# Kernel optimization log

Hardware: AMD Instinct MI355X
Metric: run time of the kernel (lower is better)

Reference implementation:

```python
import jax, jax.numpy as jnp
import numpy as np

N_HEADS = 16
DIM_HEAD = 64
ROPE_THETA = 10000.0


def _rope_tables(seq_len, dim_head, dtype):
    # [N, dim_head//2] angle tables, llama-style interleaved-pair rotation
    inv_freq = 1.0 / (ROPE_THETA ** (jnp.arange(0, dim_head, 2, dtype=jnp.float32) / dim_head))
    t = jnp.arange(seq_len, dtype=jnp.float32)
    freqs = jnp.outer(t, inv_freq)  # [N, D/2]
    return jnp.cos(freqs).astype(dtype), jnp.sin(freqs).astype(dtype)


def _apply_rope(x, cos, sin):
    # x: [B, H, N, D]; rotate interleaved pairs (x[2i], x[2i+1])
    xr = x[..., 0::2]
    xi = x[..., 1::2]
    cos = cos[None, None, :, :]
    sin = sin[None, None, :, :]
    out_r = xr * cos - xi * sin
    out_i = xr * sin + xi * cos
    return jnp.stack([out_r, out_i], axis=-1).reshape(x.shape)


def _l2norm(x, eps=1e-12):
    return x / jnp.maximum(jnp.linalg.norm(x, axis=-1, keepdims=True), eps)


def setup_inputs() -> dict:
    key = jax.random.key(0)
    ks = jax.random.split(key, 5)
    B, N, dim = 1, 4096, N_HEADS * DIM_HEAD
    q = jax.random.normal(ks[0], (B, N, dim), dtype=jnp.float32)
    k = jax.random.normal(ks[1], (B, N, dim), dtype=jnp.float32)
    v = jax.random.normal(ks[2], (B, N, dim), dtype=jnp.float32)
    qk_scale = jnp.full((1, 1, 1, DIM_HEAD), 10.0, dtype=jnp.float32)
    w_out = jax.random.normal(ks[3], (dim, dim), dtype=jnp.float32) * (dim ** -0.5)
    b_out = jnp.zeros((dim,), dtype=jnp.float32)
    return {"q": q, "k": k, "v": v, "qk_scale": qk_scale, "w_out": w_out, "b_out": b_out}


def reference(q, k, v, qk_scale, w_out, b_out):
    B, N, dim = q.shape
    H, D = N_HEADS, DIM_HEAD
    scale = D ** -0.5
    # [B, N, dim] -> [B, H, N, D]
    q = q.reshape(B, N, H, D).transpose(0, 2, 1, 3)
    k = k.reshape(B, N, H, D).transpose(0, 2, 1, 3)
    v = v.reshape(B, N, H, D).transpose(0, 2, 1, 3)
    # RoPE
    cos, sin = _rope_tables(N, D, q.dtype)
    q = _apply_rope(q, cos, sin)
    k = _apply_rope(k, cos, sin)
    # QK-norm: L2-normalize then learned scale
    q = _l2norm(q) * qk_scale
    k = _l2norm(k) * qk_scale
    # explicit attention (non-flash)
    scores = jnp.einsum('bhid,bhjd->bhij', q, k) * scale
    probs = jax.nn.softmax(scores, axis=-1)
    out = jnp.einsum('bhij,bhjd->bhid', probs, v)
    out = out.transpose(0, 2, 1, 3).reshape(B, N, dim)
    # Linear: y = x W^T + b
    return out @ w_out.T + b_out
```

## Files before the change

kernel.cpp:

```cpp
#include <hip/hip_runtime.h>
#include <hip/hip_bf16.h>

#define N_CTX 4096
#define NH    16
#define DH    64
#define DIM   1024
#define NSPLIT 2
#define KT_PER_SPLIT (N_CTX / 64 / NSPLIT)

typedef __attribute__((ext_vector_type(8))) short bf16x8;
typedef __attribute__((ext_vector_type(4))) float f32x4;

__device__ __forceinline__ ushort f2bf(float f) {
    union { float f; unsigned u; } x; x.f = f;
    unsigned r = (x.u + 0x7FFFu + ((x.u >> 16) & 1u)) >> 16;
    return (ushort)r;
}
__device__ __forceinline__ unsigned fbits(float f) {
    union { float f; unsigned u; } x; x.f = f; return x.u;
}
__device__ __forceinline__ unsigned pack_bf16(float lo, float hi) {
    unsigned a = fbits(lo) + 0x8000u;
    unsigned b = fbits(hi) + 0x8000u;
#if defined(__has_builtin)
#if __has_builtin(__builtin_amdgcn_perm)
    return __builtin_amdgcn_perm(b, a, 0x07060302u);
#else
    return (a >> 16) | (b & 0xFFFF0000u);
#endif
#else
    return (a >> 16) | (b & 0xFFFF0000u);
#endif
}
__device__ __forceinline__ float fast_exp2(float x) {
#if defined(__has_builtin)
#if __has_builtin(__builtin_amdgcn_exp2f)
    return __builtin_amdgcn_exp2f(x);
#else
    return exp2f(x);
#endif
#else
    return exp2f(x);
#endif
}

#define SC 0.18033688011112042f

__global__ __launch_bounds__(256) void prep_kernel(
    const float* __restrict__ x, const float* __restrict__ qk_scale,
    ushort* __restrict__ xb, float premul)
{
    const int lane = threadIdx.x & 63;
    const int wave = threadIdx.x >> 6;
    const int row  = blockIdx.x * 4 + wave;
    const int n = row >> 4;
    const int h = row & 15;

    float val = x[(size_t)n * DIM + h * DH + lane];
    float other = __shfl_xor(val, 1, 64);

    const int i = lane >> 1;
    float inv_freq = 1.0f / powf(10000.0f, (float)i * (1.0f / 32.0f));
    float ang = (float)n * inv_freq;
    float s, c;
    sincosf(ang, &s, &c);

    float r = (lane & 1) ? fmaf(other, s, val * c)
                         : fmaf(val, c, -(other * s));

    float ss = r * r;
    #pragma unroll
    for (int off = 32; off > 0; off >>= 1)
        ss += __shfl_xor(ss, off, 64);
    float invn = 1.0f / fmaxf(sqrtf(ss), 1e-12f);
    float scl  = qk_scale[lane] * premul;

    xb[((size_t)h * N_CTX + n) * DH + lane] = f2bf(r * invn * scl);
}

__global__ __launch_bounds__(256) void vtrans_kernel(
    const float* __restrict__ v, ushort* __restrict__ vt)
{
    __shared__ ushort L[64][68];
    const int kt = blockIdx.x, h = blockIdx.y, t = threadIdx.x;

    for (int e = t; e < 4096; e += 256) {
        int key = e >> 6, d = e & 63;
        float f = v[(size_t)(kt * 64 + key) * DIM + h * DH + d];
        L[d][key] = f2bf(f);
    }
    __syncthreads();
    for (int e = t; e < 4096; e += 256) {
        int d = e >> 6, key = e & 63;
        vt[((size_t)h * DH + d) * N_CTX + kt * 64 + key] = L[d][key];
    }
}

__global__ __launch_bounds__(256) void wconv_kernel(
    const float* __restrict__ w, ushort* __restrict__ wb)
{
    int i = (blockIdx.x * 256 + threadIdx.x) * 4;
    float4 f = *(const float4*)&w[i];
    ushort4 u;
    u.x = f2bf(f.x); u.y = f2bf(f.y); u.z = f2bf(f.z); u.w = f2bf(f.w);
    *(ushort4*)&wb[i] = u;
}

__global__ __launch_bounds__(256) void attn_kernel(
    const ushort* __restrict__ qb, const ushort* __restrict__ kb,
    const ushort* __restrict__ vt, float* __restrict__ opart,
    float* __restrict__ lpart)
{
    __shared__ ushort Ks[64][72];
    __shared__ ushort Vt[64][72];
    __shared__ ushort Ps[128][72];

    const int h     = blockIdx.y;
    const int qbase = blockIdx.x * 128;
    const int sp    = blockIdx.z;
    const int kbase = sp * (N_CTX / NSPLIT);
    const int t    = threadIdx.x;
    const int w    = t >> 6;
    const int lane = t & 63;
    const int l15  = lane & 15;
    const int quad = lane >> 4;

    bf16x8 qf[2][2];
    #pragma unroll
    for (int qt = 0; qt < 2; qt++) {
        const size_t qrow = ((size_t)h * N_CTX + qbase + w * 32 + qt * 16 + l15) * DH;
        qf[qt][0] = *(const bf16x8*)&qb[qrow + quad * 8];
        qf[qt][1] = *(const bf16x8*)&qb[qrow + 32 + quad * 8];
    }

    float l_part[2] = {0.0f, 0.0f};
    f32x4 o_acc[4][2];
    #pragma unroll
    for (int dt = 0; dt < 4; dt++)
        #pragma unroll
        for (int qt = 0; qt < 2; qt++)
            o_acc[dt][qt] = (f32x4){0.f, 0.f, 0.f, 0.f};

    const int sr = t >> 3;
    const int sc = (t & 7) * 8;
    const ushort* kp0 = &kb[((size_t)h * N_CTX + kbase + sr) * DH + sc];
    const ushort* kp1 = kp0 + (size_t)32 * DH;
    const ushort* vp0 = &vt[((size_t)h * DH + sr) * N_CTX + kbase + sc];
    const ushort* vp1 = vp0 + (size_t)32 * N_CTX;
    bf16x8 kr0 = *(const bf16x8*)kp0, kr1 = *(const bf16x8*)kp1;
    bf16x8 vr0 = *(const bf16x8*)vp0, vr1 = *(const bf16x8*)vp1;

    for (int kt = 0; kt < KT_PER_SPLIT; kt++) {
        __syncthreads();
        *(bf16x8*)&Ks[sr][sc]      = kr0;
        *(bf16x8*)&Ks[sr + 32][sc] = kr1;
        *(bf16x8*)&Vt[sr][sc]      = vr0;
        *(bf16x8*)&Vt[sr + 32][sc] = vr1;
        __syncthreads();
        if (kt + 1 < KT_PER_SPLIT) {
            kr0 = *(const bf16x8*)(kp0 + (size_t)(kt + 1) * 64 * DH);
            kr1 = *(const bf16x8*)(kp1 + (size_t)(kt + 1) * 64 * DH);
            vr0 = *(const bf16x8*)(vp0 + (size_t)(kt + 1) * 64);
            vr1 = *(const bf16x8*)(vp1 + (size_t)(kt + 1) * 64);
        }

        #pragma unroll
        for (int j = 0; j < 4; j++) {
            bf16x8 kf0 = *(const bf16x8*)&Ks[j * 16 + l15][quad * 8];
            bf16x8 kf1 = *(const bf16x8*)&Ks[j * 16 + l15][32 + quad * 8];
            f32x4 s0 = (f32x4){0.f, 0.f, 0.f, 0.f};
            f32x4 s1 = (f32x4){0.f, 0.f, 0.f, 0.f};
            s0 = __builtin_amdgcn_mfma_f32_16x16x32_bf16(kf0, qf[0][0], s0, 0, 0, 0);
            s1 = __builtin_amdgcn_mfma_f32_16x16x32_bf16(kf0, qf[1][0], s1, 0, 0, 0);
            s0 = __builtin_amdgcn_mfma_f32_16x16x32_bf16(kf1, qf[0][1], s0, 0, 0, 0);
            s1 = __builtin_amdgcn_mfma_f32_16x16x32_bf16(kf1, qf[1][1], s1, 0, 0, 0);

            {
                float p0 = fast_exp2(s0.x), p1 = fast_exp2(s0.y);
                float p2 = fast_exp2(s0.z), p3 = fast_exp2(s0.w);
                l_part[0] += (p0 + p1) + (p2 + p3);
                uint2 pk; pk.x = pack_bf16(p0, p1); pk.y = pack_bf16(p2, p3);
                *(uint2*)&Ps[w * 32 + l15][j * 16 + quad * 4] = pk;
            }
            {
                float p0 = fast_exp2(s1.x), p1 = fast_exp2(s1.y);
                float p2 = fast_exp2(s1.z), p3 = fast_exp2(s1.w);
                l_part[1] += (p0 + p1) + (p2 + p3);
                uint2 pk; pk.x = pack_bf16(p0, p1); pk.y = pack_bf16(p2, p3);
                *(uint2*)&Ps[w * 32 + 16 + l15][j * 16 + quad * 4] = pk;
            }
        }

        #pragma unroll
        for (int ks = 0; ks < 2; ks++) {
            bf16x8 pf0 = *(const bf16x8*)&Ps[w * 32 + l15][ks * 32 + quad * 8];
            bf16x8 pf1 = *(const bf16x8*)&Ps[w * 32 + 16 + l15][ks * 32 + quad * 8];
            #pragma unroll
            for (int dt = 0; dt < 4; dt++) {
                bf16x8 vf = *(const bf16x8*)&Vt[dt * 16 + l15][ks * 32 + quad * 8];
                o_acc[dt][0] = __builtin_amdgcn_mfma_f32_16x16x32_bf16(vf, pf0, o_acc[dt][0], 0, 0, 0);
                o_acc[dt][1] = __builtin_amdgcn_mfma_f32_16x16x32_bf16(vf, pf1, o_acc[dt][1], 0, 0, 0);
            }
        }
    }

    #pragma unroll
    for (int qt = 0; qt < 2; qt++) {
        float v = l_part[qt];
        v += __shfl_xor(v, 16, 64);
        v += __shfl_xor(v, 32, 64);
        if (quad == 0)
            lpart[(size_t)sp * NH * N_CTX + (size_t)h * N_CTX
                  + qbase + w * 32 + qt * 16 + l15] = v;
    }

    #pragma unroll
    for (int qt = 0; qt < 2; qt++)
        #pragma unroll
        for (int dt = 0; dt < 4; dt++) {
            f32x4 o = o_acc[dt][qt];
            float4 ov; ov.x = o.x; ov.y = o.y; ov.z = o.z; ov.w = o.w;
            *(float4*)&opart[((size_t)sp * N_CTX + qbase + w * 32 + qt * 16 + l15) * DIM
                             + h * DH + dt * 16 + quad * 4] = ov;
        }
}

__global__ __launch_bounds__(256) void combine_kernel(
    const float* __restrict__ opart, const float* __restrict__ lpart,
    ushort* __restrict__ attnb)
{
    const int idx = blockIdx.x * 256 + threadIdx.x;
    const int n   = idx >> 8;
    const int rem = idx & 255;
    const int h   = rem >> 4;
    const size_t e = (size_t)n * DIM + h * DH + (rem & 15) * 4;

    float4 o0 = *(const float4*)&opart[e];
    float4 o1 = *(const float4*)&opart[(size_t)N_CTX * DIM + e];
    float l0 = lpart[(size_t)h * N_CTX + n];
    float l1 = lpart[(size_t)NH * N_CTX + (size_t)h * N_CTX + n];
    float li = 1.0f / (l0 + l1);

    ushort4 r;
    r.x = f2bf((o0.x + o1.x) * li);
    r.y = f2bf((o0.y + o1.y) * li);
    r.z = f2bf((o0.z + o1.z) * li);
    r.w = f2bf((o0.w + o1.w) * li);
    *(ushort4*)&attnb[e] = r;
}

__global__ __launch_bounds__(256) void proj_kernel(
    const ushort* __restrict__ A, const ushort* __restrict__ W,
    const float* __restrict__ bias, float* __restrict__ out)
{
    __shared__ ushort As[128][72];
    __shared__ ushort Ws[64][72];

    const int nbase = blockIdx.x * 128;
    const int obase = blockIdx.y * 64;
    const int t    = threadIdx.x;
    const int w    = t >> 6;
    const int lane = t & 63;
    const int l15  = lane & 15;
    const int quad = lane >> 4;
    const int rw   = (w >> 1) * 64;
    const int cw   = (w & 1) * 32;

    f32x4 acc[4][2];
    #pragma unroll
    for (int mt = 0; mt < 4; mt++)
        #pragma unroll
        for (int nt = 0; nt < 2; nt++)
            acc[mt][nt] = (f32x4){0.f, 0.f, 0.f, 0.f};

    for (int kt = 0; kt < DIM / 64; kt++) {
        const int kb = kt * 64;
        __syncthreads();
        #pragma unroll
        for (int i = 0; i < 4; i++) {
            int c = t + i * 256, r = c >> 3, c8 = c & 7;
            *(bf16x8*)&As[r][c8 * 8] =
                *(const bf16x8*)&A[(size_t)(nbase + r) * DIM + kb + c8 * 8];
        }
        #pragma unroll
        for (int i = 0; i < 2; i++) {
            int c = t + i * 256, r = c >> 3, c8 = c & 7;
            *(bf16x8*)&Ws[r][c8 * 8] =
                *(const bf16x8*)&W[(size_t)(obase + r) * DIM + kb + c8 * 8];
        }
        __syncthreads();

        bf16x8 af[4][2], bfr[2][2];
        #pragma unroll
        for (int mt = 0; mt < 4; mt++)
            #pragma unroll
            for (int kh = 0; kh < 2; kh++)
                af[mt][kh] = *(const bf16x8*)&As[rw + mt * 16 + l15][kh * 32 + quad * 8];
        #pragma unroll
        for (int nt = 0; nt < 2; nt++)
            #pragma unroll
            for (int kh = 0; kh < 2; kh++)
                bfr[nt][kh] = *(const bf16x8*)&Ws[cw + nt * 16 + l15][kh * 32 + quad * 8];

        #pragma unroll
        for (int mt = 0; mt < 4; mt++)
            #pragma unroll
            for (int nt = 0; nt < 2; nt++) {
                acc[mt][nt] = __builtin_amdgcn_mfma_f32_16x16x32_bf16(af[mt][0], bfr[nt][0], acc[mt][nt], 0, 0, 0);
                acc[mt][nt] = __builtin_amdgcn_mfma_f32_16x16x32_bf16(af[mt][1], bfr[nt][1], acc[mt][nt], 0, 0, 0);
            }
    }

    #pragma unroll
    for (int nt = 0; nt < 2; nt++) {
        int o = obase + cw + nt * 16 + l15;
        float bb = bias[o];
        #pragma unroll
        for (int mt = 0; mt < 4; mt++) {
            int nrow = nbase + rw + mt * 16 + quad * 4;
            out[(size_t)(nrow + 0) * DIM + o] = acc[mt][nt].x + bb;
            out[(size_t)(nrow + 1) * DIM + o] = acc[mt][nt].y + bb;
            out[(size_t)(nrow + 2) * DIM + o] = acc[mt][nt].z + bb;
            out[(size_t)(nrow + 3) * DIM + o] = acc[mt][nt].w + bb;
        }
    }
}

extern "C" void kernel_launch(void* const* d_in, const int* in_sizes, int n_in,
                              void* d_out, int out_size, void* d_ws, size_t ws_size,
                              hipStream_t stream)
{
    const float* q        = (const float*)d_in[0];
    const float* k        = (const float*)d_in[1];
    const float* v        = (const float*)d_in[2];
    const float* qk_scale = (const float*)d_in[3];
    const float* w_out    = (const float*)d_in[4];
    const float* b_out    = (const float*)d_in[5];
    float* out = (float*)d_out;

    const size_t per = (size_t)NH * N_CTX * DH;
    ushort* qb    = (ushort*)d_ws;
    ushort* kb    = qb + per;
    ushort* vtg   = kb + per;
    ushort* attnb = vtg + per;
    ushort* wb    = attnb + per;
    float*  opart = (float*)(wb + (size_t)DIM * DIM);
    float*  lpart = opart + (size_t)NSPLIT * N_CTX * DIM;

    prep_kernel<<<dim3(N_CTX * NH / 4), 256, 0, stream>>>(q, qk_scale, qb, SC);
    prep_kernel<<<dim3(N_CTX * NH / 4), 256, 0, stream>>>(k, qk_scale, kb, 1.0f);
    vtrans_kernel<<<dim3(N_CTX / 64, NH), 256, 0, stream>>>(v, vtg);
    wconv_kernel<<<dim3(DIM * DIM / 1024), 256, 0, stream>>>(w_out, wb);
    attn_kernel<<<dim3(N_CTX / 128, NH, NSPLIT), 256, 0, stream>>>(qb, kb, vtg, opart, lpart);
    combine_kernel<<<dim3(N_CTX * DIM / 4 / 256), 256, 0, stream>>>(opart, lpart, attnb);
    proj_kernel<<<dim3(N_CTX / 128, DIM / 64), 256, 0, stream>>>(attnb, wb, b_out, out);
}
```

Measured before the change: 262.3 us.

## Load K fragments directly from global, quadruple split-K, store partials in bf16

The attention kernel stops staging K in shared memory and has each lane load its MFMA K fragments straight from global memory. It also interleaves the score/exp and PV stages per 32-key half, which shrinks the P buffer in LDS. The key split rises from two to four for more blocks in flight, and partial outputs are written as bf16 so the combine kernel reads half the bytes while summing four partials. The trade-off is more uncoalesced global K reads, extra bf16 rounding of the partial sums, and a larger combine pass.

```diff
diff --git a/kernel.cpp b/kernel.cpp
--- a/kernel.cpp
+++ b/kernel.cpp
@@ -5,7 +5,7 @@
 #define NH    16
 #define DH    64
 #define DIM   1024
-#define NSPLIT 2
+#define NSPLIT 4
 #define KT_PER_SPLIT (N_CTX / 64 / NSPLIT)
 
 typedef __attribute__((ext_vector_type(8))) short bf16x8;
@@ -15,6 +15,9 @@
     union { float f; unsigned u; } x; x.f = f;
     unsigned r = (x.u + 0x7FFFu + ((x.u >> 16) & 1u)) >> 16;
     return (ushort)r;
+}
+__device__ __forceinline__ float bf2f(ushort u) {
+    union { unsigned u; float f; } x; x.u = ((unsigned)u) << 16; return x.f;
 }
 __device__ __forceinline__ unsigned fbits(float f) {
     union { float f; unsigned u; } x; x.f = f; return x.u;
@@ -108,12 +111,11 @@
 
 __global__ __launch_bounds__(256) void attn_kernel(
     const ushort* __restrict__ qb, const ushort* __restrict__ kb,
-    const ushort* __restrict__ vt, float* __restrict__ opart,
+    const ushort* __restrict__ vt, ushort* __restrict__ opart,
     float* __restrict__ lpart)
 {
-    __shared__ ushort Ks[64][72];
     __shared__ ushort Vt[64][72];
-    __shared__ ushort Ps[128][72];
+    __shared__ ushort Ps[128][40];
 
     const int h     = blockIdx.y;
     const int qbase = blockIdx.x * 128;
@@ -143,58 +145,50 @@
 
     const int sr = t >> 3;
     const int sc = (t & 7) * 8;
-    const ushort* kp0 = &kb[((size_t)h * N_CTX + kbase + sr) * DH + sc];
-    const ushort* kp1 = kp0 + (size_t)32 * DH;
     const ushort* vp0 = &vt[((size_t)h * DH + sr) * N_CTX + kbase + sc];
     const ushort* vp1 = vp0 + (size_t)32 * N_CTX;
-    bf16x8 kr0 = *(const bf16x8*)kp0, kr1 = *(const bf16x8*)kp1;
-    bf16x8 vr0 = *(const bf16x8*)vp0, vr1 = *(const bf16x8*)vp1;
+    bf16x8 vr0 = *(const bf16x8*)vp0;
+    bf16x8 vr1 = *(const bf16x8*)vp1;
+
+    const ushort* kfp = &kb[((size_t)h * N_CTX + kbase + l15) * DH + quad * 8];
 
     for (int kt = 0; kt < KT_PER_SPLIT; kt++) {
         __syncthreads();
-        *(bf16x8*)&Ks[sr][sc]      = kr0;
-        *(bf16x8*)&Ks[sr + 32][sc] = kr1;
         *(bf16x8*)&Vt[sr][sc]      = vr0;
         *(bf16x8*)&Vt[sr + 32][sc] = vr1;
         __syncthreads();
         if (kt + 1 < KT_PER_SPLIT) {
-            kr0 = *(const bf16x8*)(kp0 + (size_t)(kt + 1) * 64 * DH);
-            kr1 = *(const bf16x8*)(kp1 + (size_t)(kt + 1) * 64 * DH);
             vr0 = *(const bf16x8*)(vp0 + (size_t)(kt + 1) * 64);
             vr1 = *(const bf16x8*)(vp1 + (size_t)(kt + 1) * 64);
         }
 
         #pragma unroll
-        for (int j = 0; j < 4; j++) {
-            bf16x8 kf0 = *(const bf16x8*)&Ks[j * 16 + l15][quad * 8];
-            bf16x8 kf1 = *(const bf16x8*)&Ks[j * 16 + l15][32 + quad * 8];
-            f32x4 s0 = (f32x4){0.f, 0.f, 0.f, 0.f};
-            f32x4 s1 = (f32x4){0.f, 0.f, 0.f, 0.f};
-            s0 = __builtin_amdgcn_mfma_f32_16x16x32_bf16(kf0, qf[0][0], s0, 0, 0, 0);
-            s1 = __builtin_amdgcn_mfma_f32_16x16x32_bf16(kf0, qf[1][0], s1, 0, 0, 0);
-            s0 = __builtin_amdgcn_mfma_f32_16x16x32_bf16(kf1, qf[0][1], s0, 0, 0, 0);
-            s1 = __builtin_amdgcn_mfma_f32_16x16x32_bf16(kf1, qf[1][1], s1, 0, 0, 0);
-
-            {
-                float p0 = fast_exp2(s0.x), p1 = fast_exp2(s0.y);
-                float p2 = fast_exp2(s0.z), p3 = fast_exp2(s0.w);
-                l_part[0] += (p0 + p1) + (p2 + p3);
-                uint2 pk; pk.x = pack_bf16(p0, p1); pk.y = pack_bf16(p2, p3);
-                *(uint2*)&Ps[w * 32 + l15][j * 16 + quad * 4] = pk;
+        for (int ks = 0; ks < 2; ks++) {
+            #pragma unroll
+            for (int jj = 0; jj < 2; jj++) {
+                const int j = ks * 2 + jj;
+                const ushort* kr = kfp + (size_t)(kt * 64 + j * 16) * DH;
+                bf16x8 kf0 = *(const bf16x8*)kr;
+                bf16x8 kf1 = *(const bf16x8*)(kr + 32);
+
+                #pragma unroll
+                for (int qt = 0; qt < 2; qt++) {
+                    f32x4 s = (f32x4){0.f, 0.f, 0.f, 0.f};
+                    s = __builtin_amdgcn_mfma_f32_16x16x32_bf16(kf0, qf[qt][0], s, 0, 0, 0);
+                    s = __builtin_amdgcn_mfma_f32_16x16x32_bf16(kf1, qf[qt][1], s, 0, 0, 0);
+
+                    float p0 = fast_exp2(s.x), p1 = fast_exp2(s.y);
+                    float p2 = fast_exp2(s.z), p3 = fast_exp2(s.w);
+                    l_part[qt] += (p0 + p1) + (p2 + p3);
+                    uint2 pk;
+                    pk.x = pack_bf16(p0, p1);
+                    pk.y = pack_bf16(p2, p3);
+                    *(uint2*)&Ps[w * 32 + qt * 16 + l15][jj * 16 + quad * 4] = pk;
+                }
             }
-            {
-                float p0 = fast_exp2(s1.x), p1 = fast_exp2(s1.y);
-                float p2 = fast_exp2(s1.z), p3 = fast_exp2(s1.w);
-                l_part[1] += (p0 + p1) + (p2 + p3);
-                uint2 pk; pk.x = pack_bf16(p0, p1); pk.y = pack_bf16(p2, p3);
-                *(uint2*)&Ps[w * 32 + 16 + l15][j * 16 + quad * 4] = pk;
-            }
-        }
-
-        #pragma unroll
-        for (int ks = 0; ks < 2; ks++) {
-            bf16x8 pf0 = *(const bf16x8*)&Ps[w * 32 + l15][ks * 32 + quad * 8];
-            bf16x8 pf1 = *(const bf16x8*)&Ps[w * 32 + 16 + l15][ks * 32 + quad * 8];
+
+            bf16x8 pf0 = *(const bf16x8*)&Ps[w * 32 + l15][quad * 8];
+            bf16x8 pf1 = *(const bf16x8*)&Ps[w * 32 + 16 + l15][quad * 8];
             #pragma unroll
             for (int dt = 0; dt < 4; dt++) {
                 bf16x8 vf = *(const bf16x8*)&Vt[dt * 16 + l15][ks * 32 + quad * 8];
@@ -219,14 +213,16 @@
         #pragma unroll
         for (int dt = 0; dt < 4; dt++) {
             f32x4 o = o_acc[dt][qt];
-            float4 ov; ov.x = o.x; ov.y = o.y; ov.z = o.z; ov.w = o.w;
-            *(float4*)&opart[((size_t)sp * N_CTX + qbase + w * 32 + qt * 16 + l15) * DIM
-                             + h * DH + dt * 16 + quad * 4] = ov;
+            ushort4 ov;
+            ov.x = f2bf(o.x); ov.y = f2bf(o.y);
+            ov.z = f2bf(o.z); ov.w = f2bf(o.w);
+            *(ushort4*)&opart[((size_t)sp * N_CTX + qbase + w * 32 + qt * 16 + l15) * DIM
+                              + h * DH + dt * 16 + quad * 4] = ov;
         }
 }
 
 __global__ __launch_bounds__(256) void combine_kernel(
-    const float* __restrict__ opart, const float* __restrict__ lpart,
+    const ushort* __restrict__ opart, const float* __restrict__ lpart,
     ushort* __restrict__ attnb)
 {
     const int idx = blockIdx.x * 256 + threadIdx.x;
@@ -235,17 +231,18 @@
     const int h   = rem >> 4;
     const size_t e = (size_t)n * DIM + h * DH + (rem & 15) * 4;
 
-    float4 o0 = *(const float4*)&opart[e];
-    float4 o1 = *(const float4*)&opart[(size_t)N_CTX * DIM + e];
-    float l0 = lpart[(size_t)h * N_CTX + n];
-    float l1 = lpart[(size_t)NH * N_CTX + (size_t)h * N_CTX + n];
-    float li = 1.0f / (l0 + l1);
+    float s0 = 0.f, s1 = 0.f, s2 = 0.f, s3 = 0.f, lsum = 0.f;
+    #pragma unroll
+    for (int sp = 0; sp < NSPLIT; sp++) {
+        ushort4 u = *(const ushort4*)&opart[(size_t)sp * N_CTX * DIM + e];
+        s0 += bf2f(u.x); s1 += bf2f(u.y); s2 += bf2f(u.z); s3 += bf2f(u.w);
+        lsum += lpart[(size_t)sp * NH * N_CTX + (size_t)h * N_CTX + n];
+    }
+    float li = 1.0f / lsum;
 
     ushort4 r;
-    r.x = f2bf((o0.x + o1.x) * li);
-    r.y = f2bf((o0.y + o1.y) * li);
-    r.z = f2bf((o0.z + o1.z) * li);
-    r.w = f2bf((o0.w + o1.w) * li);
+    r.x = f2bf(s0 * li); r.y = f2bf(s1 * li);
+    r.z = f2bf(s2 * li); r.w = f2bf(s3 * li);
     *(ushort4*)&attnb[e] = r;
 }
 
@@ -344,8 +341,8 @@
     ushort* vtg   = kb + per;
     ushort* attnb = vtg + per;
     ushort* wb    = attnb + per;
-    float*  opart = (float*)(wb + (size_t)DIM * DIM);
-    float*  lpart = opart + (size_t)NSPLIT * N_CTX * DIM;
+    ushort* opart = wb + (size_t)DIM * DIM;
+    float*  lpart = (float*)(opart + (size_t)NSPLIT * N_CTX * DIM);
 
     prep_kernel<<<dim3(N_CTX * NH / 4), 256, 0, stream>>>(q, qk_scale, qb, SC);
     prep_kernel<<<dim3(N_CTX * NH / 4), 256, 0, stream>>>(k, qk_scale, kb, 1.0f);
```

New measurement: 328.5 us. 1.25x slower.
